# Optimization experiments

Hardware: AMD Instinct MI355X
Metric: run time of the kernel (lower is better)

The kernel has to match this reference:

```python
import jax, jax.numpy as jnp
import numpy as np

B, S, D, H = 2, 2048, 1024, 16
HD = D // H  # head_dim = 64
SCALE = 1.0 / np.sqrt(np.float32(D))  # original divides by sqrt(d_keys) == sqrt(d_model)


def setup_inputs() -> dict:
    key = jax.random.key(0)
    ks = jax.random.split(key, 8)
    inp = {
        "query": jax.random.normal(ks[0], (B, S, D), jnp.float32),
        "key": jax.random.normal(ks[1], (B, S, D), jnp.float32),
        "value": jax.random.normal(ks[2], (B, S, D), jnp.float32),
        # nn.Linear weights stored as [out, in]; y = x @ W.T
        "Wq": jax.random.normal(ks[3], (D, D), jnp.float32) * 0.02,
        "Wk": jax.random.normal(ks[4], (D, D), jnp.float32) * 0.02,
        "Wv": jax.random.normal(ks[5], (D, D), jnp.float32) * 0.02,
        "Wo": jax.random.normal(ks[6], (D, D), jnp.float32) * 0.02,
        "bo": jax.random.normal(ks[7], (D,), jnp.float32) * 0.02,
    }
    return inp


def reference(query, key, value, Wq, Wk, Wv, Wo, bo):
    # projections (no bias)
    Q = jnp.einsum('bsd,ed->bse', query, Wq)
    K = jnp.einsum('bsd,ed->bse', key, Wk)
    V = jnp.einsum('bsd,ed->bse', value, Wv)
    # split heads -> [B, H, S, HD]
    Q = Q.reshape(B, S, H, HD).transpose(0, 2, 1, 3)
    K = K.reshape(B, S, H, HD).transpose(0, 2, 1, 3)
    V = V.reshape(B, S, H, HD).transpose(0, 2, 1, 3)
    # scores [B,H,S,S]; note: scaled by 1/sqrt(d_model), matching the source
    scores = jnp.einsum('bhqd,bhkd->bhqk', Q, K) * SCALE
    attn = jax.nn.softmax(scores, axis=-1)  # dropout_ratio=0 -> identity
    ctx = jnp.einsum('bhqk,bhkd->bhqd', attn, V)
    ctx = ctx.transpose(0, 2, 1, 3).reshape(B, S, D)
    return jnp.einsum('bsd,ed->bse', ctx, Wo) + bo
```

## Files before the change

kernel.cpp:

```cpp
#include <hip/hip_runtime.h>
#include <hip/hip_bf16.h>

#define B_  2
#define S_  2048
#define D_  1024
#define H_  16
#define HD_ 64
#define SCALE_ 0.03125f

typedef __bf16 bf16;
typedef __attribute__((ext_vector_type(8))) __bf16 bf16x8;
typedef __attribute__((ext_vector_type(4))) float f32x4;

__device__ __forceinline__ bf16x8 load8(const float* p) {
  const float4 a = *(const float4*)p;
  const float4 b = *(const float4*)(p + 4);
  bf16x8 r;
  r[0] = (bf16)a.x; r[1] = (bf16)a.y; r[2] = (bf16)a.z; r[3] = (bf16)a.w;
  r[4] = (bf16)b.x; r[5] = (bf16)b.y; r[6] = (bf16)b.z; r[7] = (bf16)b.w;
  return r;
}
__device__ __forceinline__ bf16x8 load8(const bf16* p) {
  return *(const bf16x8*)p;
}

__global__ __launch_bounds__(256, 2)
void gemm_qkv_kernel(const float* __restrict__ Aq, const float* __restrict__ Ak,
                     const float* __restrict__ Av, const float* __restrict__ Wq,
                     const float* __restrict__ Wk, const float* __restrict__ Wv,
                     bf16* __restrict__ Cq, bf16* __restrict__ Ck,
                     bf16* __restrict__ Cv, int M, int N, int K)
{
  __shared__ bf16 lA[128 * 32];
  __shared__ bf16 lB[128 * 32];

  const int sel = blockIdx.y >> 3;
  const int bn  = blockIdx.y & 7;
  const float* A  = sel == 0 ? Aq : (sel == 1 ? Ak : Av);
  const float* Bw = sel == 0 ? Wq : (sel == 1 ? Wk : Wv);
  bf16*        C  = sel == 0 ? Cq : (sel == 1 ? Ck : Cv);

  const int t    = threadIdx.x;
  const int wave = t >> 6;
  const int lane = t & 63;
  const int quad = lane >> 4;
  const int l16  = lane & 15;
  const int bm = blockIdx.x;
  const int wm = (wave >> 1) * 64;
  const int wn = (wave & 1) * 64;

  const int srow = t >> 2;
  const int scol = (t & 3) * 8;
  const float* gA = A  + (size_t)(bm * 128 + srow) * K + scol;
  const float* gB = Bw + (size_t)(bn * 128 + srow) * K + scol;

  f32x4 acc[4][4] = {};

  for (int k0 = 0; k0 < K; k0 += 32) {
    const bf16x8 a0 = load8(gA);
    const bf16x8 a1 = load8(gA + (size_t)64 * K);
    const bf16x8 b0 = load8(gB);
    const bf16x8 b1 = load8(gB + (size_t)64 * K);

    __syncthreads();
    *(bf16x8*)(lA + srow * 32 + scol)        = a0;
    *(bf16x8*)(lA + (srow + 64) * 32 + scol) = a1;
    *(bf16x8*)(lB + srow * 32 + scol)        = b0;
    *(bf16x8*)(lB + (srow + 64) * 32 + scol) = b1;
    __syncthreads();

    bf16x8 af[4], bfr[4];
#pragma unroll
    for (int i = 0; i < 4; ++i) {
      af[i]  = *(const bf16x8*)(lA + (wm + i * 16 + l16) * 32 + quad * 8);
      bfr[i] = *(const bf16x8*)(lB + (wn + i * 16 + l16) * 32 + quad * 8);
    }
#pragma unroll
    for (int mi = 0; mi < 4; ++mi)
#pragma unroll
      for (int ni = 0; ni < 4; ++ni)
        acc[mi][ni] = __builtin_amdgcn_mfma_f32_16x16x32_bf16(
            af[mi], bfr[ni], acc[mi][ni], 0, 0, 0);

    gA += 32;
    gB += 32;
  }

#pragma unroll
  for (int mi = 0; mi < 4; ++mi) {
#pragma unroll
    for (int ni = 0; ni < 4; ++ni) {
      const int col = bn * 128 + wn + ni * 16 + l16;
#pragma unroll
      for (int r = 0; r < 4; ++r) {
        const int row = bm * 128 + wm + mi * 16 + quad * 4 + r;
        C[(size_t)row * N + col] = (bf16)acc[mi][ni][r];
      }
    }
  }
}

__global__ __launch_bounds__(256, 2)
void gemm_out_kernel(const bf16* __restrict__ A, const float* __restrict__ Bw,
                     const float* __restrict__ bias, float* __restrict__ C,
                     int M, int N, int K)
{
  __shared__ bf16 lA[128 * 32];
  __shared__ bf16 lB[64 * 32];

  const int t    = threadIdx.x;
  const int wave = t >> 6;
  const int lane = t & 63;
  const int quad = lane >> 4;
  const int l16  = lane & 15;
  const int bm = blockIdx.x;
  const int bn = blockIdx.y;
  const int wm = wave * 32;

  const int srow = t >> 2;
  const int scol = (t & 3) * 8;
  const bf16*  gA = A  + (size_t)(bm * 128 + srow) * K + scol;
  const float* gB = Bw + (size_t)(bn * 64 + srow) * K + scol;

  f32x4 acc[2][4] = {};

  for (int k0 = 0; k0 < K; k0 += 32) {
    const bf16x8 a0 = load8(gA);
    const bf16x8 a1 = load8(gA + (size_t)64 * K);
    const bf16x8 b0 = load8(gB);

    __syncthreads();
    *(bf16x8*)(lA + srow * 32 + scol)        = a0;
    *(bf16x8*)(lA + (srow + 64) * 32 + scol) = a1;
    *(bf16x8*)(lB + srow * 32 + scol)        = b0;
    __syncthreads();

    bf16x8 af[2], bfr[4];
#pragma unroll
    for (int i = 0; i < 2; ++i)
      af[i]  = *(const bf16x8*)(lA + (wm + i * 16 + l16) * 32 + quad * 8);
#pragma unroll
    for (int i = 0; i < 4; ++i)
      bfr[i] = *(const bf16x8*)(lB + (i * 16 + l16) * 32 + quad * 8);
#pragma unroll
    for (int mi = 0; mi < 2; ++mi)
#pragma unroll
      for (int ni = 0; ni < 4; ++ni)
        acc[mi][ni] = __builtin_amdgcn_mfma_f32_16x16x32_bf16(
            af[mi], bfr[ni], acc[mi][ni], 0, 0, 0);

    gA += 32;
    gB += 32;
  }

  float bv[4];
#pragma unroll
  for (int ni = 0; ni < 4; ++ni)
    bv[ni] = bias[bn * 64 + ni * 16 + l16];
#pragma unroll
  for (int mi = 0; mi < 2; ++mi) {
#pragma unroll
    for (int ni = 0; ni < 4; ++ni) {
      const int col = bn * 64 + ni * 16 + l16;
#pragma unroll
      for (int r = 0; r < 4; ++r) {
        const int row = bm * 128 + wm + mi * 16 + quad * 4 + r;
        C[(size_t)row * N + col] = acc[mi][ni][r] + bv[ni];
      }
    }
  }
}

__global__ __launch_bounds__(256, 2)
void attn_kernel(const bf16* Q, const bf16* __restrict__ K,
                 const bf16* __restrict__ V, bf16* O)
{
  __shared__ bf16 lQ[64 * 72];
  __shared__ bf16 lK[64 * 72];
  __shared__ bf16 lVT[80 * 72];
  __shared__ bf16 lP[4][16 * 72];

  const int t    = threadIdx.x;
  const int wave = t >> 6;
  const int lane = t & 63;
  const int quad = lane >> 4;
  const int l16  = lane & 15;
  const int qt = blockIdx.x;
  const int bh = blockIdx.y;
  const size_t headoff =
      (size_t)(bh >> 4) * ((size_t)S_ * D_) + (size_t)(bh & 15) * HD_;

  for (int i = t; i < 16 * 72; i += 256) {
    const int rr = i / 72, cc = i % 72;
    lVT[(64 + rr) * 72 + cc] = (bf16)((rr == 0 && cc < 64) ? 1.0f : 0.0f);
  }

  const int sr = t >> 3;
  const int scx = (t & 7) * 8;
  {
    const bf16x8 q0 = *(const bf16x8*)(Q + headoff + (size_t)(qt * 64 + sr) * D_ + scx);
    const bf16x8 q1 = *(const bf16x8*)(Q + headoff + (size_t)(qt * 64 + sr + 32) * D_ + scx);
    *(bf16x8*)(lQ + sr * 72 + scx)        = q0;
    *(bf16x8*)(lQ + (sr + 32) * 72 + scx) = q1;
  }
  __syncthreads();

  bf16x8 qf[2];
  {
    const int row = wave * 16 + l16;
#pragma unroll
    for (int ks = 0; ks < 2; ++ks)
      qf[ks] = *(const bf16x8*)(lQ + row * 72 + (ks * 4 + quad) * 8);
  }

  f32x4 acco[4] = {};
  f32x4 acc4 = {};

  const int vd  = t & 63;
  const int vkg = t >> 6;

  for (int kt = 0; kt < S_ / 64; ++kt) {
    __syncthreads();

    {
      const bf16x8 k0 = *(const bf16x8*)(K + headoff + (size_t)(kt * 64 + sr) * D_ + scx);
      const bf16x8 k1 = *(const bf16x8*)(K + headoff + (size_t)(kt * 64 + sr + 32) * D_ + scx);
      *(bf16x8*)(lK + sr * 72 + scx)        = k0;
      *(bf16x8*)(lK + (sr + 32) * 72 + scx) = k1;
    }
    {
      const bf16* gv = V + headoff + (size_t)(kt * 64 + vkg * 16) * D_ + vd;
      bf16 tmp[16];
#pragma unroll
      for (int j = 0; j < 16; ++j) tmp[j] = gv[(size_t)j * D_];
      bf16x8 w0, w1;
#pragma unroll
      for (int j = 0; j < 8; ++j) { w0[j] = tmp[j]; w1[j] = tmp[8 + j]; }
      *(bf16x8*)(lVT + vd * 72 + vkg * 16)     = w0;
      *(bf16x8*)(lVT + vd * 72 + vkg * 16 + 8) = w1;
    }
    __syncthreads();

    f32x4 sc[4] = {};
#pragma unroll
    for (int nt = 0; nt < 4; ++nt) {
#pragma unroll
      for (int ks = 0; ks < 2; ++ks) {
        const int krow = nt * 16 + l16;
        const bf16x8 kf = *(const bf16x8*)(lK + krow * 72 + (ks * 4 + quad) * 8);
        sc[nt] = __builtin_amdgcn_mfma_f32_16x16x32_bf16(qf[ks], kf, sc[nt], 0, 0, 0);
      }
    }

    bf16* lPw = lP[wave];
#pragma unroll
    for (int nt = 0; nt < 4; ++nt) {
#pragma unroll
      for (int r = 0; r < 4; ++r) {
        const float p = __expf(sc[nt][r] * SCALE_);
        lPw[(quad * 4 + r) * 72 + nt * 16 + l16] = (bf16)p;
      }
    }

    bf16x8 pf[2];
#pragma unroll
    for (int ks = 0; ks < 2; ++ks)
      pf[ks] = *(const bf16x8*)(lPw + l16 * 72 + ks * 32 + quad * 8);
#pragma unroll
    for (int dt = 0; dt < 4; ++dt) {
#pragma unroll
      for (int ks = 0; ks < 2; ++ks) {
        const bf16x8 vf =
            *(const bf16x8*)(lVT + (dt * 16 + l16) * 72 + ks * 32 + quad * 8);
        acco[dt] = __builtin_amdgcn_mfma_f32_16x16x32_bf16(pf[ks], vf, acco[dt], 0, 0, 0);
      }
    }
#pragma unroll
    for (int ks = 0; ks < 2; ++ks) {
      const bf16x8 vf1 =
          *(const bf16x8*)(lVT + (64 + l16) * 72 + ks * 32 + quad * 8);
      acc4 = __builtin_amdgcn_mfma_f32_16x16x32_bf16(pf[ks], vf1, acc4, 0, 0, 0);
    }
  }

  float den[4];
#pragma unroll
  for (int r = 0; r < 4; ++r)
    den[r] = 1.f / __shfl(acc4[r], lane & 48);
#pragma unroll
  for (int dt = 0; dt < 4; ++dt) {
#pragma unroll
    for (int r = 0; r < 4; ++r) {
      const int row = qt * 64 + wave * 16 + quad * 4 + r;
      const int d   = dt * 16 + l16;
      O[headoff + (size_t)row * D_ + d] = (bf16)(acco[dt][r] * den[r]);
    }
  }
}

extern "C" void kernel_launch(void* const* d_in, const int* in_sizes, int n_in,
                              void* d_out, int out_size, void* d_ws, size_t ws_size,
                              hipStream_t stream)
{
  const float* q  = (const float*)d_in[0];
  const float* k  = (const float*)d_in[1];
  const float* v  = (const float*)d_in[2];
  const float* Wq = (const float*)d_in[3];
  const float* Wk = (const float*)d_in[4];
  const float* Wv = (const float*)d_in[5];
  const float* Wo = (const float*)d_in[6];
  const float* bo = (const float*)d_in[7];
  float* outf = (float*)d_out;
  bf16*  outs = (bf16*)d_out;
  bf16*  wsb  = (bf16*)d_ws;

  const size_t SD = (size_t)S_ * D_;
  const size_t MD = (size_t)B_ * S_ * D_;

  dim3 blk(256);

  if (ws_size >= MD * sizeof(bf16)) {
    bf16* Kp = outs;
    bf16* Vp = outs + MD;
    bf16* Qp = wsb;

    dim3 gqkv(B_ * S_ / 128, 24);
    dim3 gattn(S_ / 64, B_ * H_);
    dim3 gout(B_ * S_ / 128, D_ / 64);

    gemm_qkv_kernel<<<gqkv, blk, 0, stream>>>(q, k, v, Wq, Wk, Wv,
                                              Qp, Kp, Vp, B_ * S_, D_, D_);
    attn_kernel<<<gattn, blk, 0, stream>>>(Qp, Kp, Vp, Qp);
    gemm_out_kernel<<<gout, blk, 0, stream>>>(Qp, Wo, bo, outf,
                                              B_ * S_, D_, D_);
  } else {
    dim3 gqkv(S_ / 128, 24);
    dim3 gattn(S_ / 64, H_);
    dim3 gout(S_ / 128, D_ / 64);

    for (int b = 0; b < B_; ++b) {
      const size_t o = (size_t)b * SD;
      bf16* Kp = outs + b * MD;
      bf16* Vp = outs + b * MD + SD;
      bf16* Qp = wsb;

      gemm_qkv_kernel<<<gqkv, blk, 0, stream>>>(q + o, k + o, v + o,
                                                Wq, Wk, Wv,
                                                Qp, Kp, Vp, S_, D_, D_);
      attn_kernel<<<gattn, blk, 0, stream>>>(Qp, Kp, Vp, Qp);
      gemm_out_kernel<<<gout, blk, 0, stream>>>(Qp, Wo, bo, outf + o,
                                                S_, D_, D_);
    }
  }
}
```

Before: 252.0 us.

## Pre-convert weights to bf16, use direct-to-LDS loads, prefetch K/V, remap attention grid

Adds a kernel that converts all four weight matrices to bf16 once per call, so the projection GEMMs can stream B tiles straight into LDS with global_load_lds instead of converting fp32 in registers. Folds the softmax scale into the Q projection epilogue. In attention it register-prefetches the next K/V tile while the current tile computes, loads V as paired 32-bit words for the transpose, and remaps block indices so blocks of the same head run together. The extra conversion pass and larger workspace need are the added costs, and the old per-batch fallback path is removed.

```diff
diff --git a/kernel.cpp b/kernel.cpp
--- a/kernel.cpp
+++ b/kernel.cpp
@@ -10,7 +10,16 @@
 
 typedef __bf16 bf16;
 typedef __attribute__((ext_vector_type(8))) __bf16 bf16x8;
+typedef __attribute__((ext_vector_type(8))) unsigned short u16x8;
+typedef __attribute__((ext_vector_type(4))) __bf16 bf16x4;
 typedef __attribute__((ext_vector_type(4))) float f32x4;
+
+__device__ __forceinline__ void gload_lds16(const void* g, void* l) {
+  __builtin_amdgcn_global_load_lds(
+      (const __attribute__((address_space(1))) unsigned int*)g,
+      (__attribute__((address_space(3))) unsigned int*)l,
+      16, 0, 0);
+}
 
 __device__ __forceinline__ bf16x8 load8(const float* p) {
   const float4 a = *(const float4*)p;
@@ -24,12 +33,25 @@
   return *(const bf16x8*)p;
 }
 
+__global__ __launch_bounds__(256)
+void wconv_kernel(const float* __restrict__ Wq, const float* __restrict__ Wk,
+                  const float* __restrict__ Wv, const float* __restrict__ Wo,
+                  bf16* __restrict__ dst)
+{
+  const int n4  = (blockIdx.x * 256 + threadIdx.x) * 4;
+  const int m   = n4 >> 20;
+  const int off = n4 & ((1 << 20) - 1);
+  const float* src = m == 0 ? Wq : (m == 1 ? Wk : (m == 2 ? Wv : Wo));
+  const float4 a = *(const float4*)(src + off);
+  bf16x4 o = {(bf16)a.x, (bf16)a.y, (bf16)a.z, (bf16)a.w};
+  *(bf16x4*)(dst + n4) = o;
+}
+
 __global__ __launch_bounds__(256, 2)
-void gemm_qkv_kernel(const float* __restrict__ Aq, const float* __restrict__ Ak,
-                     const float* __restrict__ Av, const float* __restrict__ Wq,
-                     const float* __restrict__ Wk, const float* __restrict__ Wv,
-                     bf16* __restrict__ Cq, bf16* __restrict__ Ck,
-                     bf16* __restrict__ Cv, int M, int N, int K)
+void gemm_qkv_b_kernel(const float* __restrict__ Aq, const float* __restrict__ Ak,
+                       const float* __restrict__ Av, const bf16* __restrict__ Wb,
+                       bf16* __restrict__ Cq, bf16* __restrict__ Ck,
+                       bf16* __restrict__ Cv)
 {
   __shared__ bf16 lA[128 * 32];
   __shared__ bf16 lB[128 * 32];
@@ -37,8 +59,9 @@
   const int sel = blockIdx.y >> 3;
   const int bn  = blockIdx.y & 7;
   const float* A  = sel == 0 ? Aq : (sel == 1 ? Ak : Av);
-  const float* Bw = sel == 0 ? Wq : (sel == 1 ? Wk : Wv);
+  const bf16*  Bw = Wb + ((size_t)sel << 20);
   bf16*        C  = sel == 0 ? Cq : (sel == 1 ? Ck : Cv);
+  const float scale = sel == 0 ? SCALE_ : 1.0f;
 
   const int t    = threadIdx.x;
   const int wave = t >> 6;
@@ -51,22 +74,20 @@
 
   const int srow = t >> 2;
   const int scol = (t & 3) * 8;
-  const float* gA = A  + (size_t)(bm * 128 + srow) * K + scol;
-  const float* gB = Bw + (size_t)(bn * 128 + srow) * K + scol;
+  const float* gA  = A  + (size_t)(bm * 128 + srow) * D_ + scol;
+  const bf16*  gBb = Bw + (size_t)(bn * 128 + srow) * D_ + scol;
 
   f32x4 acc[4][4] = {};
 
-  for (int k0 = 0; k0 < K; k0 += 32) {
+  for (int k0 = 0; k0 < D_; k0 += 32) {
     const bf16x8 a0 = load8(gA);
-    const bf16x8 a1 = load8(gA + (size_t)64 * K);
-    const bf16x8 b0 = load8(gB);
-    const bf16x8 b1 = load8(gB + (size_t)64 * K);
+    const bf16x8 a1 = load8(gA + (size_t)64 * D_);
 
     __syncthreads();
     *(bf16x8*)(lA + srow * 32 + scol)        = a0;
     *(bf16x8*)(lA + (srow + 64) * 32 + scol) = a1;
-    *(bf16x8*)(lB + srow * 32 + scol)        = b0;
-    *(bf16x8*)(lB + (srow + 64) * 32 + scol) = b1;
+    gload_lds16(gBb,                   (char*)lB + wave * 1024);
+    gload_lds16(gBb + (size_t)64 * D_, (char*)lB + 4096 + wave * 1024);
     __syncthreads();
 
     bf16x8 af[4], bfr[4];
@@ -82,8 +103,8 @@
         acc[mi][ni] = __builtin_amdgcn_mfma_f32_16x16x32_bf16(
             af[mi], bfr[ni], acc[mi][ni], 0, 0, 0);
 
-    gA += 32;
-    gB += 32;
+    gA  += 32;
+    gBb += 32;
   }
 
 #pragma unroll
@@ -94,16 +115,15 @@
 #pragma unroll
       for (int r = 0; r < 4; ++r) {
         const int row = bm * 128 + wm + mi * 16 + quad * 4 + r;
-        C[(size_t)row * N + col] = (bf16)acc[mi][ni][r];
+        C[(size_t)row * D_ + col] = (bf16)(acc[mi][ni][r] * scale);
       }
     }
   }
 }
 
 __global__ __launch_bounds__(256, 2)
-void gemm_out_kernel(const bf16* __restrict__ A, const float* __restrict__ Bw,
-                     const float* __restrict__ bias, float* __restrict__ C,
-                     int M, int N, int K)
+void gemm_out_b_kernel(const bf16* __restrict__ A, const bf16* __restrict__ Bw,
+                       const float* __restrict__ bias, float* __restrict__ C)
 {
   __shared__ bf16 lA[128 * 32];
   __shared__ bf16 lB[64 * 32];
@@ -119,20 +139,16 @@
 
   const int srow = t >> 2;
   const int scol = (t & 3) * 8;
-  const bf16*  gA = A  + (size_t)(bm * 128 + srow) * K + scol;
-  const float* gB = Bw + (size_t)(bn * 64 + srow) * K + scol;
+  const bf16* gA = A  + (size_t)(bm * 128 + srow) * D_ + scol;
+  const bf16* gB = Bw + (size_t)(bn * 64 + srow) * D_ + scol;
 
   f32x4 acc[2][4] = {};
 
-  for (int k0 = 0; k0 < K; k0 += 32) {
-    const bf16x8 a0 = load8(gA);
-    const bf16x8 a1 = load8(gA + (size_t)64 * K);
-    const bf16x8 b0 = load8(gB);
-
-    __syncthreads();
-    *(bf16x8*)(lA + srow * 32 + scol)        = a0;
-    *(bf16x8*)(lA + (srow + 64) * 32 + scol) = a1;
-    *(bf16x8*)(lB + srow * 32 + scol)        = b0;
+  for (int k0 = 0; k0 < D_; k0 += 32) {
+    __syncthreads();
+    gload_lds16(gA,                   (char*)lA + wave * 1024);
+    gload_lds16(gA + (size_t)64 * D_, (char*)lA + 4096 + wave * 1024);
+    gload_lds16(gB,                   (char*)lB + wave * 1024);
     __syncthreads();
 
     bf16x8 af[2], bfr[4];
@@ -165,28 +181,177 @@
 #pragma unroll
       for (int r = 0; r < 4; ++r) {
         const int row = bm * 128 + wm + mi * 16 + quad * 4 + r;
-        C[(size_t)row * N + col] = acc[mi][ni][r] + bv[ni];
+        C[(size_t)row * D_ + col] = acc[mi][ni][r] + bv[ni];
       }
     }
   }
 }
 
 __global__ __launch_bounds__(256, 2)
-void attn_kernel(const bf16* Q, const bf16* __restrict__ K,
-                 const bf16* __restrict__ V, bf16* O)
-{
-  __shared__ bf16 lQ[64 * 72];
-  __shared__ bf16 lK[64 * 72];
-  __shared__ bf16 lVT[80 * 72];
-  __shared__ bf16 lP[4][16 * 72];
+void gemm_qkv_kernel(const float* __restrict__ Aq, const float* __restrict__ Ak,
+                     const float* __restrict__ Av, const float* __restrict__ Wq,
+                     const float* __restrict__ Wk, const float* __restrict__ Wv,
+                     bf16* __restrict__ Cq, bf16* __restrict__ Ck,
+                     bf16* __restrict__ Cv)
+{
+  __shared__ bf16 lA[128 * 32];
+  __shared__ bf16 lB[128 * 32];
+
+  const int sel = blockIdx.y >> 3;
+  const int bn  = blockIdx.y & 7;
+  const float* A  = sel == 0 ? Aq : (sel == 1 ? Ak : Av);
+  const float* Bw = sel == 0 ? Wq : (sel == 1 ? Wk : Wv);
+  bf16*        C  = sel == 0 ? Cq : (sel == 1 ? Ck : Cv);
+  const float scale = sel == 0 ? SCALE_ : 1.0f;
 
   const int t    = threadIdx.x;
   const int wave = t >> 6;
   const int lane = t & 63;
   const int quad = lane >> 4;
   const int l16  = lane & 15;
-  const int qt = blockIdx.x;
-  const int bh = blockIdx.y;
+  const int bm = blockIdx.x;
+  const int wm = (wave >> 1) * 64;
+  const int wn = (wave & 1) * 64;
+
+  const int srow = t >> 2;
+  const int scol = (t & 3) * 8;
+  const float* gA = A  + (size_t)(bm * 128 + srow) * D_ + scol;
+  const float* gB = Bw + (size_t)(bn * 128 + srow) * D_ + scol;
+
+  f32x4 acc[4][4] = {};
+
+  for (int k0 = 0; k0 < D_; k0 += 32) {
+    const bf16x8 a0 = load8(gA);
+    const bf16x8 a1 = load8(gA + (size_t)64 * D_);
+    const bf16x8 b0 = load8(gB);
+    const bf16x8 b1 = load8(gB + (size_t)64 * D_);
+
+    __syncthreads();
+    *(bf16x8*)(lA + srow * 32 + scol)        = a0;
+    *(bf16x8*)(lA + (srow + 64) * 32 + scol) = a1;
+    *(bf16x8*)(lB + srow * 32 + scol)        = b0;
+    *(bf16x8*)(lB + (srow + 64) * 32 + scol) = b1;
+    __syncthreads();
+
+    bf16x8 af[4], bfr[4];
+#pragma unroll
+    for (int i = 0; i < 4; ++i) {
+      af[i]  = *(const bf16x8*)(lA + (wm + i * 16 + l16) * 32 + quad * 8);
+      bfr[i] = *(const bf16x8*)(lB + (wn + i * 16 + l16) * 32 + quad * 8);
+    }
+#pragma unroll
+    for (int mi = 0; mi < 4; ++mi)
+#pragma unroll
+      for (int ni = 0; ni < 4; ++ni)
+        acc[mi][ni] = __builtin_amdgcn_mfma_f32_16x16x32_bf16(
+            af[mi], bfr[ni], acc[mi][ni], 0, 0, 0);
+
+    gA += 32;
+    gB += 32;
+  }
+
+#pragma unroll
+  for (int mi = 0; mi < 4; ++mi) {
+#pragma unroll
+    for (int ni = 0; ni < 4; ++ni) {
+      const int col = bn * 128 + wn + ni * 16 + l16;
+#pragma unroll
+      for (int r = 0; r < 4; ++r) {
+        const int row = bm * 128 + wm + mi * 16 + quad * 4 + r;
+        C[(size_t)row * D_ + col] = (bf16)(acc[mi][ni][r] * scale);
+      }
+    }
+  }
+}
+
+__global__ __launch_bounds__(256, 2)
+void gemm_out_kernel(const bf16* __restrict__ A, const float* __restrict__ Bw,
+                     const float* __restrict__ bias, float* __restrict__ C)
+{
+  __shared__ bf16 lA[128 * 32];
+  __shared__ bf16 lB[64 * 32];
+
+  const int t    = threadIdx.x;
+  const int wave = t >> 6;
+  const int lane = t & 63;
+  const int quad = lane >> 4;
+  const int l16  = lane & 15;
+  const int bm = blockIdx.x;
+  const int bn = blockIdx.y;
+  const int wm = wave * 32;
+
+  const int srow = t >> 2;
+  const int scol = (t & 3) * 8;
+  const bf16*  gA = A  + (size_t)(bm * 128 + srow) * D_ + scol;
+  const float* gB = Bw + (size_t)(bn * 64 + srow) * D_ + scol;
+
+  f32x4 acc[2][4] = {};
+
+  for (int k0 = 0; k0 < D_; k0 += 32) {
+    const bf16x8 a0 = load8(gA);
+    const bf16x8 a1 = load8(gA + (size_t)64 * D_);
+    const bf16x8 b0 = load8(gB);
+
+    __syncthreads();
+    *(bf16x8*)(lA + srow * 32 + scol)        = a0;
+    *(bf16x8*)(lA + (srow + 64) * 32 + scol) = a1;
+    *(bf16x8*)(lB + srow * 32 + scol)        = b0;
+    __syncthreads();
+
+    bf16x8 af[2], bfr[4];
+#pragma unroll
+    for (int i = 0; i < 2; ++i)
+      af[i]  = *(const bf16x8*)(lA + (wm + i * 16 + l16) * 32 + quad * 8);
+#pragma unroll
+    for (int i = 0; i < 4; ++i)
+      bfr[i] = *(const bf16x8*)(lB + (i * 16 + l16) * 32 + quad * 8);
+#pragma unroll
+    for (int mi = 0; mi < 2; ++mi)
+#pragma unroll
+      for (int ni = 0; ni < 4; ++ni)
+        acc[mi][ni] = __builtin_amdgcn_mfma_f32_16x16x32_bf16(
+            af[mi], bfr[ni], acc[mi][ni], 0, 0, 0);
+
+    gA += 32;
+    gB += 32;
+  }
+
+  float bv[4];
+#pragma unroll
+  for (int ni = 0; ni < 4; ++ni)
+    bv[ni] = bias[bn * 64 + ni * 16 + l16];
+#pragma unroll
+  for (int mi = 0; mi < 2; ++mi) {
+#pragma unroll
+    for (int ni = 0; ni < 4; ++ni) {
+      const int col = bn * 64 + ni * 16 + l16;
+#pragma unroll
+      for (int r = 0; r < 4; ++r) {
+        const int row = bm * 128 + wm + mi * 16 + quad * 4 + r;
+        C[(size_t)row * D_ + col] = acc[mi][ni][r] + bv[ni];
+      }
+    }
+  }
+}
+
+__global__ __launch_bounds__(256, 2)
+void attn_kernel(const bf16* Q, const bf16* __restrict__ K,
+                 const bf16* __restrict__ V, bf16* O)
+{
+  __shared__ bf16 lQ[64 * 72];
+  __shared__ bf16 lK[64 * 72];
+  __shared__ bf16 lVT[80 * 72];
+  __shared__ bf16 lP[4][16 * 72];
+
+  const int t    = threadIdx.x;
+  const int wave = t >> 6;
+  const int lane = t & 63;
+  const int quad = lane >> 4;
+  const int l16  = lane & 15;
+
+  const int flat = blockIdx.y * 32 + blockIdx.x;
+  const int qt   = (flat >> 3) & 31;
+  const int bh   = (flat & 7) * 4 + (flat >> 8);
   const size_t headoff =
       (size_t)(bh >> 4) * ((size_t)S_ * D_) + (size_t)(bh & 15) * HD_;
 
@@ -195,7 +360,7 @@
     lVT[(64 + rr) * 72 + cc] = (bf16)((rr == 0 && cc < 64) ? 1.0f : 0.0f);
   }
 
-  const int sr = t >> 3;
+  const int sr  = t >> 3;
   const int scx = (t & 7) * 8;
   {
     const bf16x8 q0 = *(const bf16x8*)(Q + headoff + (size_t)(qt * 64 + sr) * D_ + scx);
@@ -216,30 +381,47 @@
   f32x4 acco[4] = {};
   f32x4 acc4 = {};
 
-  const int vd  = t & 63;
-  const int vkg = t >> 6;
+  const int dp = t & 31;
+  const int kg = t >> 5;
+
+  bf16x8 pk0, pk1;
+  unsigned int pv[8];
+  {
+    const bf16* kb = K + headoff + (size_t)(sr) * D_ + scx;
+    pk0 = load8(kb);
+    pk1 = load8(kb + (size_t)32 * D_);
+    const bf16* vb = V + headoff + (size_t)(kg * 8) * D_ + 2 * dp;
+#pragma unroll
+    for (int j = 0; j < 8; ++j)
+      pv[j] = *(const unsigned int*)(vb + (size_t)j * D_);
+  }
 
   for (int kt = 0; kt < S_ / 64; ++kt) {
     __syncthreads();
 
+    *(bf16x8*)(lK + sr * 72 + scx)        = pk0;
+    *(bf16x8*)(lK + (sr + 32) * 72 + scx) = pk1;
     {
-      const bf16x8 k0 = *(const bf16x8*)(K + headoff + (size_t)(kt * 64 + sr) * D_ + scx);
-      const bf16x8 k1 = *(const bf16x8*)(K + headoff + (size_t)(kt * 64 + sr + 32) * D_ + scx);
-      *(bf16x8*)(lK + sr * 72 + scx)        = k0;
-      *(bf16x8*)(lK + (sr + 32) * 72 + scx) = k1;
-    }
-    {
-      const bf16* gv = V + headoff + (size_t)(kt * 64 + vkg * 16) * D_ + vd;
-      bf16 tmp[16];
-#pragma unroll
-      for (int j = 0; j < 16; ++j) tmp[j] = gv[(size_t)j * D_];
-      bf16x8 w0, w1;
-#pragma unroll
-      for (int j = 0; j < 8; ++j) { w0[j] = tmp[j]; w1[j] = tmp[8 + j]; }
-      *(bf16x8*)(lVT + vd * 72 + vkg * 16)     = w0;
-      *(bf16x8*)(lVT + vd * 72 + vkg * 16 + 8) = w1;
-    }
-    __syncthreads();
+      u16x8 w0, w1;
+#pragma unroll
+      for (int j = 0; j < 8; ++j) {
+        w0[j] = (unsigned short)(pv[j] & 0xffffu);
+        w1[j] = (unsigned short)(pv[j] >> 16);
+      }
+      *(u16x8*)(lVT + (2 * dp) * 72 + kg * 8)     = w0;
+      *(u16x8*)(lVT + (2 * dp + 1) * 72 + kg * 8) = w1;
+    }
+    __syncthreads();
+
+    if (kt + 1 < S_ / 64) {
+      const bf16* kb = K + headoff + (size_t)((kt + 1) * 64 + sr) * D_ + scx;
+      pk0 = load8(kb);
+      pk1 = load8(kb + (size_t)32 * D_);
+      const bf16* vb = V + headoff + (size_t)((kt + 1) * 64 + kg * 8) * D_ + 2 * dp;
+#pragma unroll
+      for (int j = 0; j < 8; ++j)
+        pv[j] = *(const unsigned int*)(vb + (size_t)j * D_);
+    }
 
     f32x4 sc[4] = {};
 #pragma unroll
@@ -257,7 +439,7 @@
     for (int nt = 0; nt < 4; ++nt) {
 #pragma unroll
       for (int r = 0; r < 4; ++r) {
-        const float p = __expf(sc[nt][r] * SCALE_);
+        const float p = __expf(sc[nt][r]);
         lPw[(quad * 4 + r) * 72 + nt * 16 + l16] = (bf16)p;
       }
     }
@@ -318,38 +500,28 @@
   const size_t MD = (size_t)B_ * S_ * D_;
 
   dim3 blk(256);
-
-  if (ws_size >= MD * sizeof(bf16)) {
-    bf16* Kp = outs;
-    bf16* Vp = outs + MD;
+  dim3 gqkv(B_ * S_ / 128, 24);
+  dim3 gattn(S_ / 64, B_ * H_);
+  dim3 gout(B_ * S_ / 128, D_ / 64);
+
+  bf16* Kp = outs;
+  bf16* Vp = outs + MD;
+
+  if (ws_size >= (size_t)16 << 20) {
+    bf16* Wb = wsb;
+    bf16* Qp = wsb + MD;
+
+    wconv_kernel<<<4096, blk, 0, stream>>>(Wq, Wk, Wv, Wo, Wb);
+    gemm_qkv_b_kernel<<<gqkv, blk, 0, stream>>>(q, k, v, Wb, Qp, Kp, Vp);
+    attn_kernel<<<gattn, blk, 0, stream>>>(Qp, Kp, Vp, Qp);
+    gemm_out_b_kernel<<<gout, blk, 0, stream>>>(Qp, Wb + 3 * ((size_t)1 << 20),
+                                                bo, outf);
+  } else {
     bf16* Qp = wsb;
 
-    dim3 gqkv(B_ * S_ / 128, 24);
-    dim3 gattn(S_ / 64, B_ * H_);
-    dim3 gout(B_ * S_ / 128, D_ / 64);
-
     gemm_qkv_kernel<<<gqkv, blk, 0, stream>>>(q, k, v, Wq, Wk, Wv,
-                                              Qp, Kp, Vp, B_ * S_, D_, D_);
+                                              Qp, Kp, Vp);
     attn_kernel<<<gattn, blk, 0, stream>>>(Qp, Kp, Vp, Qp);
-    gemm_out_kernel<<<gout, blk, 0, stream>>>(Qp, Wo, bo, outf,
-                                              B_ * S_, D_, D_);
-  } else {
-    dim3 gqkv(S_ / 128, 24);
-    dim3 gattn(S_ / 64, H_);
-    dim3 gout(S_ / 128, D_ / 64);
-
-    for (int b = 0; b < B_; ++b) {
-      const size_t o = (size_t)b * SD;
-      bf16* Kp = outs + b * MD;
-      bf16* Vp = outs + b * MD + SD;
-      bf16* Qp = wsb;
-
-      gemm_qkv_kernel<<<gqkv, blk, 0, stream>>>(q + o, k + o, v + o,
-                                                Wq, Wk, Wv,
-                                                Qp, Kp, Vp, S_, D_, D_);
-      attn_kernel<<<gattn, blk, 0, stream>>>(Qp, Kp, Vp, Qp);
-      gemm_out_kernel<<<gout, blk, 0, stream>>>(Qp, Wo, bo, outf + o,
-                                                S_, D_, D_);
-    }
-  }
-}
+    gemm_out_kernel<<<gout, blk, 0, stream>>>(Qp, Wo, bo, outf);
+  }
+}
```

Measured after the change: 245.4 us. -2.6%, faster.
